# Kernel tuning notes

Hardware: AMD Instinct MI355X
Metric: run time of the kernel (lower is better)

## Reference

```python
import jax, jax.numpy as jnp
import numpy as np

NEG = -65504.0  # torch.finfo(float16).min
EPS = 1e-6

B, T, D = 2, 1024, 2048
H, HD = 16, 128          # n_head, head_dim
K = 128                  # dynamic_w_hidden_dim
IH = 1                   # dynamic_hidden_dim = H // squeeze_ratio


def _rope(x, freqs_cis):
    # x: [B,T,H,hd]; 'half' mode: first/second half are the rotation pair,
    # output is interleaved (stack(...,-1).flatten(3) in torch).
    half = x.shape[-1] // 2
    a, b = x[..., :half], x[..., half:]
    cos = freqs_cis[None, :, None, :, 0]
    sin = freqs_cis[None, :, None, :, 1]
    out = jnp.stack([a * cos - b * sin, b * cos + a * sin], axis=-1)
    return out.reshape(x.shape)


def _cross_head_proj(inputs, qw1, qw2, kw1, kw2, qdd, kdd):
    # inputs: [B,N,T,S]; qw1/qw2: [B,T,I,N]; kw1/kw2: [B,S,I,N]; qdd: [B,T,N]; kdd: [B,S,N]
    out = inputs
    out = out + jnp.einsum('bnts,btin,btim->bmts', inputs, qw1, qw2)
    out = out + jnp.einsum('bnts,bsin,bsim->bmts', inputs, kw1, kw2)
    out = out + inputs * jnp.swapaxes(qdd, 1, 2)[..., None]   # [B,N,T,1]
    out = out + inputs * jnp.swapaxes(kdd, 1, 2)[:, :, None, :]  # [B,N,1,S]
    return out


def setup_inputs() -> dict:
    key = jax.random.key(0)
    ks = jax.random.split(key, 7)
    x = jax.random.normal(ks[0], (B, T, D), jnp.float32)
    mask = jnp.tril(jnp.ones((1, 1, T, T), bool))  # causal
    # rotary tables: [T, hd/2, 2] (cos, sin)
    inv = 1.0 / (10000.0 ** (jnp.arange(0, HD, 2, dtype=jnp.float32) / HD))
    ang = jnp.arange(T, dtype=jnp.float32)[:, None] * inv[None, :]
    freqs_cis = jnp.stack([jnp.cos(ang), jnp.sin(ang)], axis=-1)
    s = 0.02
    wqkv = jax.random.normal(ks[1], (D, 3 * H * HD), jnp.float32) * s
    wo = jax.random.normal(ks[2], (H * HD, D), jnp.float32) * s
    dw1 = jax.random.normal(ks[3], (D, 4, K), jnp.float32) * s
    qkw = jax.random.normal(ks[4], (4, K, 2 * IH, H), jnp.float32) * s
    dd_w = jax.random.normal(ks[5], (D, 4 * H), jnp.float32) * s
    return {"x": x, "mask": mask, "freqs_cis": freqs_cis, "wqkv": wqkv,
            "wo": wo, "dw1": dw1, "qkw": qkw, "dd_w": dd_w}


def reference(x, mask, freqs_cis, wqkv, wo, dw1, qkw, dd_w):
    b, t, d = x.shape
    qkv = x @ wqkv
    q, k, v = jnp.split(qkv, [H * HD, 2 * H * HD], axis=-1)
    q = q.reshape(b, t, H, HD)
    k = k.reshape(b, t, H, HD)
    v = v.reshape(b, t, H, HD)
    q = _rope(q, freqs_cis)
    k = _rope(k, freqs_cis)
    q = jnp.swapaxes(q, 1, 2) * (HD ** -0.5)  # [B,H,T,hd]
    k = jnp.swapaxes(k, 1, 2)
    v = jnp.swapaxes(v, 1, 2)

    # ---- DynamicWeightProjection (G=1, squeezed) ----
    dw_hidden = jax.nn.gelu(jnp.einsum('btd,dck->btck', x, dw1), approximate=False)
    w = jnp.einsum('btck,ckim->btcim', dw_hidden, qkw)  # [B,T,4,2*IH,H]
    w1, w2 = w[..., :IH, :], w[..., IH:, :]
    w1 = w1 * jax.lax.rsqrt(jnp.mean(w1 * w1, axis=-1, keepdims=True) + EPS)
    pre_qw1, pre_kw1, post_qw1, post_kw1 = [w1[:, :, i] for i in range(4)]
    pre_qw2, pre_kw2, post_qw2, post_kw2 = [w2[:, :, i] for i in range(4)]
    dd = jnp.tanh(x @ dd_w).reshape(b, t, 4, H)
    pre_qdd, pre_kdd, post_qdd, post_kdd = [dd[:, :, i] for i in range(4)]

    # ---- attention with cross-head mixing ----
    logits = jnp.einsum('bhtd,bhsd->bhts', q, k)
    logits = _cross_head_proj(logits, pre_qw1, pre_qw2, pre_kw1, pre_kw2, pre_qdd, pre_kdd)
    logits = jnp.where(mask, logits, NEG)
    probs = jax.nn.softmax(logits, axis=-1)
    probs = _cross_head_proj(probs, post_qw1, post_qw2, post_kw1, post_kw2, post_qdd, post_kdd)
    o = jnp.einsum('bhts,bhsd->bhtd', probs, v)
    o = jnp.swapaxes(o, 1, 2).reshape(b, t, H * HD)
    return o @ wo
```

## Files before the change

kernel.cpp:

```cpp
#include <hip/hip_runtime.h>


typedef unsigned short u16;
typedef unsigned int u32;
typedef __attribute__((ext_vector_type(8))) short s16x8;
typedef __attribute__((ext_vector_type(4))) float f32x4;
typedef __attribute__((ext_vector_type(2))) float f32x2;
typedef __attribute__((ext_vector_type(2))) u16 u16x2;
typedef __attribute__((ext_vector_type(8))) u16 u16x8;

#define DEV __device__ __forceinline__

DEV float bf2f(u16 u) { union { u32 u; float f; } a; a.u = ((u32)u) << 16; return a.f; }
DEV u16 f2bf(float f) {
  union { float f; u32 u; } a; a.f = f;
  u32 r = a.u + 0x7fffu + ((a.u >> 16) & 1u);
  return (u16)(r >> 16);
}

DEV void gload16(const void* g, void* l) {
  __builtin_amdgcn_global_load_lds((__attribute__((address_space(1))) void*)g,
                                   (__attribute__((address_space(3))) void*)l,
                                   16, 0, 0);
}

template <int OUTBF>
__global__ __launch_bounds__(512, 1) void gemm256(
    const u16* __restrict__ A, const u16* __restrict__ B, void* __restrict__ Cp,
    int K, int lda, int ldb, int ldc)
{
  __shared__ u16 sA[2][256 * 64];
  __shared__ u16 sB[2][256 * 64];
  const int tid = threadIdx.x, ln = tid & 63;
  const int wid = tid >> 6, wm = wid >> 2, wn = wid & 3;

  const int nx = gridDim.x;
  const int fid = blockIdx.y * nx + blockIdx.x;
  const int cpx = (nx * gridDim.y) >> 3;
  const int nid = (fid & 7) * cpx + (fid >> 3);
  const int bx = nid % nx, by = nid / nx;

  const u16* Ab = A + (size_t)(by * 256) * lda;
  const u16* Bb = B + (size_t)(bx * 256) * ldb;

  f32x4 acc[8][4];
#pragma unroll
  for (int m = 0; m < 8; ++m)
#pragma unroll
    for (int n = 0; n < 4; ++n) {
      f32x4 zz = {0.f, 0.f, 0.f, 0.f};
      acc[m][n] = zz;
    }

  int srow[4], scol[4], soff[4];
#pragma unroll
  for (int i = 0; i < 4; ++i) {
    int o = i * 8192 + tid * 16;
    soff[i] = o;
    int r = o >> 7;
    srow[i] = r;
    scol[i] = ((o & 127) ^ ((r & 7) << 4)) >> 1;
  }

#define STAGE256(ba, bb, k0)                                              \
  {                                                                       \
    _Pragma("unroll")                                                     \
    for (int i_ = 0; i_ < 4; ++i_)                                        \
      gload16(Ab + (size_t)srow[i_] * lda + (k0) + scol[i_],              \
              (char*)(ba) + soff[i_]);                                    \
    _Pragma("unroll")                                                     \
    for (int i_ = 0; i_ < 4; ++i_)                                        \
      gload16(Bb + (size_t)srow[i_] * ldb + (k0) + scol[i_],              \
              (char*)(bb) + soff[i_]);                                    \
  }

  const int arow = wm * 128 + (ln & 15);
  const int brow = wn * 64 + (ln & 15);
  const int kb = (ln >> 4) * 16;
  const int frswz = (ln & 7) << 4;
  const int NT = K >> 6;

  STAGE256(sA[0], sB[0], 0);
  if (NT > 1) STAGE256(sA[1], sB[1], 64);

  for (int t = 0; t < NT; ++t) {
    const int c = t & 1;
    asm volatile("s_waitcnt vmcnt(8)" ::: "memory");
    __builtin_amdgcn_s_barrier();
    const char* pa = (const char*)sA[c];
    const char* pb = (const char*)sB[c];
    s16x8 bfr[4][2];
#pragma unroll
    for (int ph = 0; ph < 4; ++ph) {
      if (ph == 0) {
#pragma unroll
        for (int n = 0; n < 4; ++n)
#pragma unroll
          for (int kk = 0; kk < 2; ++kk)
            bfr[n][kk] = *(const s16x8*)(pb + (size_t)(brow + n * 16) * 128 + ((kk * 64 + kb) ^ frswz));
      }
      s16x8 afr[2][2];
#pragma unroll
      for (int mm = 0; mm < 2; ++mm)
#pragma unroll
        for (int kk = 0; kk < 2; ++kk)
          afr[mm][kk] = *(const s16x8*)(pa + (size_t)(arow + (ph * 2 + mm) * 16) * 128 + ((kk * 64 + kb) ^ frswz));
      __builtin_amdgcn_s_barrier();
      __builtin_amdgcn_s_setprio(1);
#pragma unroll
      for (int mm = 0; mm < 2; ++mm)
#pragma unroll
        for (int n = 0; n < 4; ++n)
#pragma unroll
          for (int kk = 0; kk < 2; ++kk)
            acc[ph * 2 + mm][n] = __builtin_amdgcn_mfma_f32_16x16x32_bf16(
                afr[mm][kk], bfr[n][kk], acc[ph * 2 + mm][n], 0, 0, 0);
      __builtin_amdgcn_s_setprio(0);
    }
    __builtin_amdgcn_s_barrier();
    if (t + 2 < NT) STAGE256(sA[c], sB[c], (t + 2) * 64);
  }
#undef STAGE256

  const int r0 = by * 256 + wm * 128 + ((ln >> 4) << 2);
  const int c0 = bx * 256 + wn * 64 + (ln & 15);
#pragma unroll
  for (int m = 0; m < 8; ++m)
#pragma unroll
    for (int n = 0; n < 4; ++n)
#pragma unroll
      for (int j = 0; j < 4; ++j) {
        int row = r0 + m * 16 + j, col = c0 + n * 16;
        if (OUTBF)
          ((u16*)Cp)[(size_t)row * ldc + col] = f2bf(acc[m][n][j]);
        else
          ((float*)Cp)[(size_t)row * ldc + col] = acc[m][n][j];
      }
}

template <int OUTBF>
__global__ __launch_bounds__(256) void gemm_bt(
    const u16* __restrict__ A, const u16* __restrict__ B, void* __restrict__ Cp,
    int K, int lda, int ldb, int ldc,
    long sAb, long sBb, long sCb1, long sCb2, int CZ2, int cmode, int swz)
{
  int bx = blockIdx.x, by = blockIdx.y;
  if (swz) {
    int nx = gridDim.x;
    int fid = by * nx + bx;
    int cpx = (nx * gridDim.y) >> 3;
    int nid = (fid & 7) * cpx + (fid >> 3);
    bx = nid % nx; by = nid / nx;
  }
  if (cmode == 1 && bx > by) return;
  __shared__ u16 sA[128 * 64];
  __shared__ u16 sB[128 * 64];
  const int tid = threadIdx.x, wv = tid >> 6, ln = tid & 63;
  const int z = blockIdx.z;
  const u16* Ab = A + (size_t)z * sAb + (size_t)(by * 128) * lda;
  const u16* Bb = B + (size_t)z * sBb + (size_t)(bx * 128) * ldb;
  const int wr = (wv >> 1) * 64, wc = (wv & 1) * 64;
  const int Keff = (cmode == 2) ? min(K, (by + 1) * 128) : K;

  f32x4 acc[4][4];
#pragma unroll
  for (int m = 0; m < 4; ++m)
#pragma unroll
    for (int n = 0; n < 4; ++n) {
      f32x4 zz = {0.f, 0.f, 0.f, 0.f};
      acc[m][n] = zz;
    }

  int o_[4], r_[4], cb_[4];
#pragma unroll
  for (int i = 0; i < 4; ++i) {
    int o = (wv * 4 + i) * 1024 + ln * 16;
    o_[i] = o;
    int r = o >> 7;
    r_[i] = r;
    cb_[i] = (o & 127) ^ ((r & 7) << 4);
  }
  const int frswz = (ln & 7) << 4;
  const int fkcol = (ln >> 4) << 4;

  for (int k0 = 0; k0 < Keff; k0 += 64) {
    __syncthreads();
#pragma unroll
    for (int i = 0; i < 4; ++i)
      gload16(Ab + (size_t)r_[i] * lda + (k0 + (cb_[i] >> 1)), (char*)sA + o_[i]);
#pragma unroll
    for (int i = 0; i < 4; ++i)
      gload16(Bb + (size_t)r_[i] * ldb + (k0 + (cb_[i] >> 1)), (char*)sB + o_[i]);
    __syncthreads();

#pragma unroll
    for (int ks = 0; ks < 2; ++ks) {
      s16x8 av[4], bv[4];
#pragma unroll
      for (int m = 0; m < 4; ++m) {
        int row = wr + m * 16 + (ln & 15);
        int addr = row * 128 + ((ks * 64 + fkcol) ^ frswz);
        av[m] = *(const s16x8*)((const char*)sA + addr);
      }
#pragma unroll
      for (int n = 0; n < 4; ++n) {
        int row = wc + n * 16 + (ln & 15);
        int addr = row * 128 + ((ks * 64 + fkcol) ^ frswz);
        bv[n] = *(const s16x8*)((const char*)sB + addr);
      }
#pragma unroll
      for (int m = 0; m < 4; ++m)
#pragma unroll
        for (int n = 0; n < 4; ++n)
          acc[m][n] = __builtin_amdgcn_mfma_f32_16x16x32_bf16(av[m], bv[n], acc[m][n], 0, 0, 0);
    }
  }

  const size_t cbase = (size_t)(z / CZ2) * sCb1 + (size_t)(z % CZ2) * sCb2;
  const int r0 = by * 128 + wr + ((ln >> 4) << 2);
  const int c0 = bx * 128 + wc + (ln & 15);
#pragma unroll
  for (int m = 0; m < 4; ++m)
#pragma unroll
    for (int n = 0; n < 4; ++n)
#pragma unroll
      for (int j = 0; j < 4; ++j) {
        int row = r0 + m * 16 + j, col = c0 + n * 16;
        if (OUTBF)
          ((u16*)Cp)[cbase + (size_t)row * ldc + col] = f2bf(acc[m][n][j]);
        else
          ((float*)Cp)[cbase + (size_t)row * ldc + col] = acc[m][n][j];
      }
}

template <int INBF>
__global__ __launch_bounds__(256) void transpose_to_bf16(
    const void* __restrict__ srcv, u16* __restrict__ dst,
    int R, int C, int Cpad, int srcLd, long sSrc1, long sSrc2, int Z2, long sDst)
{
  __shared__ float tile[32][33];
  const int z = blockIdx.z, z1 = z / Z2, z2 = z % Z2;
  const size_t sbase = (size_t)z1 * sSrc1 + (size_t)z2 * sSrc2;
  u16* d = dst + (size_t)z * sDst;
  const int c0 = blockIdx.x * 32, r0 = blockIdx.y * 32;
  const int tx = threadIdx.x, ty = threadIdx.y;
#pragma unroll
  for (int i = 0; i < 4; ++i) {
    int r = r0 + ty + i * 8, c = c0 + tx;
    float v = 0.f;
    if (c < C && r < R) {
      if (INBF) v = bf2f(((const u16*)srcv)[sbase + (size_t)r * srcLd + c]);
      else      v = ((const float*)srcv)[sbase + (size_t)r * srcLd + c];
    }
    tile[ty + i * 8][tx] = v;
  }
  __syncthreads();
#pragma unroll
  for (int i = 0; i < 4; ++i) {
    int dr = c0 + ty + i * 8, dc = r0 + tx;
    if (dr < Cpad && dc < R) d[(size_t)dr * R + dc] = f2bf(tile[tx][ty + i * 8]);
  }
}

__global__ void cvt_f32_bf16_k(const float* __restrict__ src, u16* __restrict__ dst, int n4) {
  int i = blockIdx.x * 256 + threadIdx.x;
  if (i >= n4) return;
  const float4 v = ((const float4*)src)[i];
  u16* o = dst + (size_t)i * 4;
  o[0] = f2bf(v.x); o[1] = f2bf(v.y); o[2] = f2bf(v.z); o[3] = f2bf(v.w);
}

__global__ __launch_bounds__(256) void rope_k(
    const u16* __restrict__ qkvm, const float* __restrict__ fc,
    u16* __restrict__ qb, u16* __restrict__ kb)
{
  const int bt = blockIdx.x, b = bt >> 10, t = bt & 1023;
  const u16* row = qkvm + (size_t)bt * 6912;
  const float SC = 0.08838834764831845f;
#pragma unroll
  for (int it = 0; it < 4; ++it) {
    int idx = threadIdx.x + it * 256;
    int h = idx >> 6, j = idx & 63;
    float c = fc[(t * 64 + j) * 2], sn = fc[(t * 64 + j) * 2 + 1];
    float qa = bf2f(row[h * 128 + j]), qbv = bf2f(row[h * 128 + 64 + j]);
    float ka = bf2f(row[2048 + h * 128 + j]), kbv = bf2f(row[2048 + h * 128 + 64 + j]);
    size_t o = ((size_t)(b * 16 + h) * 1024 + t) * 128 + 2 * j;
    qb[o]     = f2bf((qa * c - qbv * sn) * SC);
    qb[o + 1] = f2bf((qbv * c + qa * sn) * SC);
    kb[o]     = f2bf(ka * c - kbv * sn);
    kb[o + 1] = f2bf(kbv * c + ka * sn);
  }
}

__global__ __launch_bounds__(64) void gelu_bf16_k(u16* __restrict__ qm) {
  int bt = blockIdx.x, tid = threadIdx.x;
  u16* p = qm + (size_t)bt * 6912 + 6144 + tid * 8;
  u16x8 v = *(u16x8*)p;
#pragma unroll
  for (int i = 0; i < 8; ++i) {
    float f = bf2f(v[i]);
    f = 0.5f * f * (1.f + erff(f * 0.70710678118654752f));
    v[i] = f2bf(f);
  }
  *(u16x8*)p = v;
}

__global__ __launch_bounds__(64) void wproj_k(
    const u16* __restrict__ qkvm, const float* __restrict__ qkw,
    float* __restrict__ w1a, float* __restrict__ w2a, float* __restrict__ kpT)
{
  const int bt = blockIdx.x, ln = threadIdx.x;
  const int c = ln >> 4, m = ln & 15;
  const int b = bt >> 10, t = bt & 1023;
  const u16* hp = qkvm + (size_t)bt * 6912 + 6144 + c * 128;
  const float* Wp = qkw + (size_t)c * 4096 + m;
  float w1 = 0.f, w2 = 0.f;
  for (int k = 0; k < 128; ++k) {
    float hv = bf2f(hp[k]);
    w1 += hv * Wp[k * 32];
    w2 += hv * Wp[k * 32 + 16];
  }
  float ss = w1 * w1;
  ss += __shfl_xor(ss, 1); ss += __shfl_xor(ss, 2);
  ss += __shfl_xor(ss, 4); ss += __shfl_xor(ss, 8);
  float nrm = rsqrtf(ss * (1.f / 16.f) + 1e-6f);
  float w1n = w1 * nrm;
  size_t o = (size_t)bt * 64 + c * 16 + m;
  w1a[o] = w1n;
  w2a[o] = w2;
  size_t kb = (size_t)b * 98304 + (size_t)m * 1024 + t;
  if (c == 1) { kpT[kb] = w1n; kpT[kb + 16384] = w2; }
  if (c == 3) { kpT[kb + 49152] = w1n; kpT[kb + 65536] = w2; }
}

__global__ __launch_bounds__(64) void dd_k(const u16* __restrict__ qkvm,
                                           float* __restrict__ dda, float* __restrict__ kpT) {
  int bt = blockIdx.x, ln = threadIdx.x;
  int c = ln >> 4, m = ln & 15;
  int b = bt >> 10, t = bt & 1023;
  float v = tanhf(bf2f(qkvm[(size_t)bt * 6912 + 6656 + ln]));
  dda[(size_t)bt * 64 + ln] = v;
  size_t kb = (size_t)b * 98304 + (size_t)m * 1024 + t;
  if (c == 1) kpT[kb + 32768] = v;
  if (c == 3) kpT[kb + 81920] = v;
}

__global__ __launch_bounds__(512, 4) void proj_softmax_k(
    const float* __restrict__ L, u16* __restrict__ P,
    const float* __restrict__ w1a, const float* __restrict__ w2a,
    const float* __restrict__ dda, const float* __restrict__ kparT)
{
  const int t = blockIdx.x, b = blockIdx.y;
  const int tid = threadIdx.x, wv = tid >> 6, ln = tid & 63;
  const int s0 = tid * 2;
  const bool live = (s0 <= t);

  __shared__ float qpar[6][16];
  __shared__ float red2[16][8];
  __shared__ float rzf[16];
  if (tid < 96) {
    int a = tid >> 4, hh = tid & 15;
    const float* sp = (a == 0 || a == 3) ? w1a : ((a == 1 || a == 4) ? w2a : dda);
    int cc = (a < 3) ? 0 : 2;
    qpar[a][hh] = sp[(size_t)(b * 1024 + t) * 64 + cc * 16 + hh];
  }
  __syncthreads();

  const float* kp = kparT + (size_t)b * 98304 + s0;
  float v[16][2];
  const size_t lbase = ((size_t)(b * 16) * 1024 + t) * 1024 + s0;

  if (live) {
#pragma unroll
    for (int h = 0; h < 16; ++h) {
      f32x2 d = *(const f32x2*)(L + lbase + (size_t)h * 1048576);
      v[h][0] = d[0]; v[h][1] = d[1];
    }
    float dq0 = 0.f, dq1 = 0.f, dk0 = 0.f, dk1 = 0.f;
#pragma unroll
    for (int h = 0; h < 16; ++h) {
      f32x2 k1 = *(const f32x2*)(kp + h * 1024);
      dq0 += v[h][0] * qpar[0][h]; dq1 += v[h][1] * qpar[0][h];
      dk0 += v[h][0] * k1[0];      dk1 += v[h][1] * k1[1];
    }
    const bool ok1 = (s0 + 1 <= t);
#pragma unroll
    for (int h = 0; h < 16; ++h) {
      f32x2 k2 = *(const f32x2*)(kp + 16384 + h * 1024);
      f32x2 kd = *(const f32x2*)(kp + 32768 + h * 1024);
      float a0 = v[h][0] * (1.f + qpar[2][h] + kd[0]) + qpar[1][h] * dq0 + k2[0] * dk0;
      float a1 = v[h][1] * (1.f + qpar[2][h] + kd[1]) + qpar[1][h] * dq1 + k2[1] * dk1;
      v[h][0] = __expf(a0);
      v[h][1] = ok1 ? __expf(a1) : 0.f;
    }
  }

#pragma unroll
  for (int h = 0; h < 16; ++h) {
    float x = live ? (v[h][0] + v[h][1]) : 0.f;
#pragma unroll
    for (int off = 32; off > 0; off >>= 1) x += __shfl_xor(x, off);
    if (ln == 0) red2[h][wv] = x;
  }
  __syncthreads();
  if (tid < 16)
    rzf[tid] = 1.f / (((red2[tid][0] + red2[tid][1]) + (red2[tid][2] + red2[tid][3])) +
                      ((red2[tid][4] + red2[tid][5]) + (red2[tid][6] + red2[tid][7])));
  __syncthreads();

  const size_t pbase = ((size_t)(b * 16) * 1024 + t) * 1024 + s0;
  if (live) {
    float pdq0 = 0.f, pdq1 = 0.f, pdk0 = 0.f, pdk1 = 0.f;
#pragma unroll
    for (int h = 0; h < 16; ++h) {
      float rz = rzf[h];
      f32x2 k1 = *(const f32x2*)(kp + 49152 + h * 1024);
      float p0 = v[h][0] * rz, p1 = v[h][1] * rz;
      v[h][0] = p0; v[h][1] = p1;
      pdq0 += p0 * qpar[3][h]; pdq1 += p1 * qpar[3][h];
      pdk0 += p0 * k1[0];      pdk1 += p1 * k1[1];
    }
#pragma unroll
    for (int h = 0; h < 16; ++h) {
      f32x2 k2 = *(const f32x2*)(kp + 65536 + h * 1024);
      f32x2 kd = *(const f32x2*)(kp + 81920 + h * 1024);
      u16x2 pk;
      pk[0] = f2bf(v[h][0] * (1.f + qpar[5][h] + kd[0]) + qpar[4][h] * pdq0 + k2[0] * pdk0);
      pk[1] = f2bf(v[h][1] * (1.f + qpar[5][h] + kd[1]) + qpar[4][h] * pdq1 + k2[1] * pdk1);
      *(u16x2*)(P + pbase + (size_t)h * 1048576) = pk;
    }
  } else {
    u16x2 z2 = {0, 0};
#pragma unroll
    for (int h = 0; h < 16; ++h)
      *(u16x2*)(P + pbase + (size_t)h * 1048576) = z2;
  }
}

extern "C" void kernel_launch(void* const* d_in, const int* in_sizes, int n_in,
                              void* d_out, int out_size, void* d_ws, size_t ws_size,
                              hipStream_t stream)
{
  (void)in_sizes; (void)n_in; (void)out_size; (void)ws_size;
  const float* x    = (const float*)d_in[0];
  const float* fc   = (const float*)d_in[2];
  const float* wqkv = (const float*)d_in[3];
  const float* wo   = (const float*)d_in[4];
  const float* dw1  = (const float*)d_in[5];
  const float* qkw  = (const float*)d_in[6];
  const float* ddw  = (const float*)d_in[7];
  float* out = (float*)d_out;
  char* w = (char*)d_ws;

  u16*   woT   = (u16*)(w + 0);
  u16*   qb    = (u16*)(w + 8388608);
  u16*   kb    = (u16*)(w + 16777216);
  u16*   vT    = (u16*)(w + 25165824);
  u16*   obf   = (u16*)(w + 33554432);
  float* w1a   = (float*)(w + 41943040);
  float* w2a   = (float*)(w + 42467328);
  float* dda   = (float*)(w + 42991616);
  const size_t TB = 43515904;
  u16*   xb    = (u16*)(w + TB);
  u16*   wallT = (u16*)(w + TB + 8388608);
  u16*   qkvm  = (u16*)(w + TB + 36700160);
  float* L     = (float*)(w + TB);
  u16*   P     = (u16*)(w + TB + 134217728);
  float* kparT = (float*)(w + 244842496);

  cvt_f32_bf16_k<<<4096, 256, 0, stream>>>(x, xb, 1048576);
  transpose_to_bf16<0><<<dim3(192, 64, 1), dim3(32, 8), 0, stream>>>(wqkv, wallT, 2048, 6144, 6144, 6144, 0, 0, 1, 0);
  transpose_to_bf16<0><<<dim3(16, 64, 1),  dim3(32, 8), 0, stream>>>(dw1,  wallT + (size_t)6144 * 2048, 2048, 512, 512, 512, 0, 0, 1, 0);
  transpose_to_bf16<0><<<dim3(8, 64, 1),   dim3(32, 8), 0, stream>>>(ddw,  wallT + (size_t)6656 * 2048, 2048, 64, 256, 64, 0, 0, 1, 0);
  transpose_to_bf16<0><<<dim3(64, 64, 1),  dim3(32, 8), 0, stream>>>(wo,   woT, 2048, 2048, 2048, 2048, 0, 0, 1, 0);

  gemm256<1><<<dim3(27, 8, 1), 512, 0, stream>>>(xb, wallT, qkvm, 2048, 2048, 2048, 6912);
  rope_k<<<2048, 256, 0, stream>>>(qkvm, fc, qb, kb);
  transpose_to_bf16<1><<<dim3(4, 32, 32), dim3(32, 8), 0, stream>>>(qkvm + 4096, vT, 1024, 128, 128, 6912, 7077888, 128, 16, 131072);

  gelu_bf16_k<<<2048, 64, 0, stream>>>(qkvm);
  wproj_k<<<2048, 64, 0, stream>>>(qkvm, qkw, w1a, w2a, kparT);
  dd_k<<<2048, 64, 0, stream>>>(qkvm, dda, kparT);

  gemm_bt<0><<<dim3(8, 8, 32), 256, 0, stream>>>(qb, kb, L, 128, 128, 128, 1024, 131072, 131072, 1048576, 0, 1, 1, 0);
  proj_softmax_k<<<dim3(1024, 2, 1), 512, 0, stream>>>(L, P, w1a, w2a, dda, kparT);
  gemm_bt<1><<<dim3(1, 8, 32), 256, 0, stream>>>(P, vT, obf, 1024, 1024, 1024, 2048, 1048576, 131072, 2097152, 128, 16, 2, 0);

  gemm_bt<0><<<dim3(16, 16, 1), 256, 0, stream>>>(obf, woT, out, 2048, 2048, 2048, 2048, 0, 0, 0, 0, 1, 0, 1);
}
```

Before: 318.6 us.

## Store attention logits in bf16 and retile QKV GEMM to 1024 threads

The Q·K^T logits buffer now holds bf16 instead of fp32, which halves the write traffic of the logits GEMM and the read traffic of the cross-head softmax kernel. The softmax kernel converts the values back to float on load, so the logits carry less precision before the cross-head mixing and softmax. Separately, the fused QKV projection GEMM goes from 512 to 1024 threads with 16 waves, each owning a 64x64 sub-tile. Its A and B tile loads are split and staggered across phases, trading per-wave register pressure for more waves in flight.

Measured after the change: 295.2 us, median of 2. 1.08x faster.

```diff
diff --git a/kernel.cpp b/kernel.cpp
--- a/kernel.cpp
+++ b/kernel.cpp
@@ -25,7 +25,7 @@
 }
 
 template <int OUTBF>
-__global__ __launch_bounds__(512, 1) void gemm256(
+__global__ __launch_bounds__(1024, 1) void gemm256(
     const u16* __restrict__ A, const u16* __restrict__ B, void* __restrict__ Cp,
     int K, int lda, int ldb, int ldc)
 {
@@ -43,49 +43,52 @@
   const u16* Ab = A + (size_t)(by * 256) * lda;
   const u16* Bb = B + (size_t)(bx * 256) * ldb;
 
-  f32x4 acc[8][4];
-#pragma unroll
-  for (int m = 0; m < 8; ++m)
+  f32x4 acc[4][4];
+#pragma unroll
+  for (int m = 0; m < 4; ++m)
 #pragma unroll
     for (int n = 0; n < 4; ++n) {
       f32x4 zz = {0.f, 0.f, 0.f, 0.f};
       acc[m][n] = zz;
     }
 
-  int srow[4], scol[4], soff[4];
-#pragma unroll
-  for (int i = 0; i < 4; ++i) {
-    int o = i * 8192 + tid * 16;
+  int srow[2], scol[2], soff[2];
+#pragma unroll
+  for (int i = 0; i < 2; ++i) {
+    int o = i * 16384 + tid * 16;
     soff[i] = o;
     int r = o >> 7;
     srow[i] = r;
     scol[i] = ((o & 127) ^ ((r & 7) << 4)) >> 1;
   }
 
-#define STAGE256(ba, bb, k0)                                              \
+#define STAGE_A(ba, k0)                                                   \
   {                                                                       \
     _Pragma("unroll")                                                     \
-    for (int i_ = 0; i_ < 4; ++i_)                                        \
+    for (int i_ = 0; i_ < 2; ++i_)                                        \
       gload16(Ab + (size_t)srow[i_] * lda + (k0) + scol[i_],              \
               (char*)(ba) + soff[i_]);                                    \
+  }
+#define STAGE_B(bb, k0)                                                   \
+  {                                                                       \
     _Pragma("unroll")                                                     \
-    for (int i_ = 0; i_ < 4; ++i_)                                        \
+    for (int i_ = 0; i_ < 2; ++i_)                                        \
       gload16(Bb + (size_t)srow[i_] * ldb + (k0) + scol[i_],              \
               (char*)(bb) + soff[i_]);                                    \
   }
 
-  const int arow = wm * 128 + (ln & 15);
+  const int arow = wm * 64 + (ln & 15);
   const int brow = wn * 64 + (ln & 15);
   const int kb = (ln >> 4) * 16;
   const int frswz = (ln & 7) << 4;
   const int NT = K >> 6;
 
-  STAGE256(sA[0], sB[0], 0);
-  if (NT > 1) STAGE256(sA[1], sB[1], 64);
+  STAGE_A(sA[0], 0); STAGE_B(sB[0], 0);
+  STAGE_A(sA[1], 64); STAGE_B(sB[1], 64);
 
   for (int t = 0; t < NT; ++t) {
     const int c = t & 1;
-    asm volatile("s_waitcnt vmcnt(8)" ::: "memory");
+    asm volatile("s_waitcnt vmcnt(4)" ::: "memory");
     __builtin_amdgcn_s_barrier();
     const char* pa = (const char*)sA[c];
     const char* pb = (const char*)sB[c];
@@ -99,33 +102,31 @@
           for (int kk = 0; kk < 2; ++kk)
             bfr[n][kk] = *(const s16x8*)(pb + (size_t)(brow + n * 16) * 128 + ((kk * 64 + kb) ^ frswz));
       }
-      s16x8 afr[2][2];
-#pragma unroll
-      for (int mm = 0; mm < 2; ++mm)
+      s16x8 afr[2];
+#pragma unroll
+      for (int kk = 0; kk < 2; ++kk)
+        afr[kk] = *(const s16x8*)(pa + (size_t)(arow + ph * 16) * 128 + ((kk * 64 + kb) ^ frswz));
+      __builtin_amdgcn_s_barrier();
+      if (ph == 1 && t + 2 < NT) STAGE_B(sB[c], (t + 2) * 64);
+      __builtin_amdgcn_s_setprio(1);
+#pragma unroll
+      for (int n = 0; n < 4; ++n)
 #pragma unroll
         for (int kk = 0; kk < 2; ++kk)
-          afr[mm][kk] = *(const s16x8*)(pa + (size_t)(arow + (ph * 2 + mm) * 16) * 128 + ((kk * 64 + kb) ^ frswz));
-      __builtin_amdgcn_s_barrier();
-      __builtin_amdgcn_s_setprio(1);
-#pragma unroll
-      for (int mm = 0; mm < 2; ++mm)
-#pragma unroll
-        for (int n = 0; n < 4; ++n)
-#pragma unroll
-          for (int kk = 0; kk < 2; ++kk)
-            acc[ph * 2 + mm][n] = __builtin_amdgcn_mfma_f32_16x16x32_bf16(
-                afr[mm][kk], bfr[n][kk], acc[ph * 2 + mm][n], 0, 0, 0);
+          acc[ph][n] = __builtin_amdgcn_mfma_f32_16x16x32_bf16(
+              afr[kk], bfr[n][kk], acc[ph][n], 0, 0, 0);
       __builtin_amdgcn_s_setprio(0);
     }
     __builtin_amdgcn_s_barrier();
-    if (t + 2 < NT) STAGE256(sA[c], sB[c], (t + 2) * 64);
-  }
-#undef STAGE256
-
-  const int r0 = by * 256 + wm * 128 + ((ln >> 4) << 2);
+    if (t + 2 < NT) STAGE_A(sA[c], (t + 2) * 64);
+  }
+#undef STAGE_A
+#undef STAGE_B
+
+  const int r0 = by * 256 + wm * 64 + ((ln >> 4) << 2);
   const int c0 = bx * 256 + wn * 64 + (ln & 15);
 #pragma unroll
-  for (int m = 0; m < 8; ++m)
+  for (int m = 0; m < 4; ++m)
 #pragma unroll
     for (int n = 0; n < 4; ++n)
 #pragma unroll
@@ -346,7 +347,7 @@
 }
 
 __global__ __launch_bounds__(512, 4) void proj_softmax_k(
-    const float* __restrict__ L, u16* __restrict__ P,
+    const u16* __restrict__ L, u16* __restrict__ P,
     const float* __restrict__ w1a, const float* __restrict__ w2a,
     const float* __restrict__ dda, const float* __restrict__ kparT)
 {
@@ -373,8 +374,8 @@
   if (live) {
 #pragma unroll
     for (int h = 0; h < 16; ++h) {
-      f32x2 d = *(const f32x2*)(L + lbase + (size_t)h * 1048576);
-      v[h][0] = d[0]; v[h][1] = d[1];
+      u16x2 d = *(const u16x2*)(L + lbase + (size_t)h * 1048576);
+      v[h][0] = bf2f(d[0]); v[h][1] = bf2f(d[1]);
     }
     float dq0 = 0.f, dq1 = 0.f, dk0 = 0.f, dk1 = 0.f;
 #pragma unroll
@@ -464,8 +465,8 @@
   u16*   xb    = (u16*)(w + TB);
   u16*   wallT = (u16*)(w + TB + 8388608);
   u16*   qkvm  = (u16*)(w + TB + 36700160);
-  float* L     = (float*)(w + TB);
-  u16*   P     = (u16*)(w + TB + 134217728);
+  u16*   L     = (u16*)(w + TB);
+  u16*   P     = (u16*)(w + TB + 67108864);
   float* kparT = (float*)(w + 244842496);
 
   cvt_f32_bf16_k<<<4096, 256, 0, stream>>>(x, xb, 1048576);
@@ -474,7 +475,7 @@
   transpose_to_bf16<0><<<dim3(8, 64, 1),   dim3(32, 8), 0, stream>>>(ddw,  wallT + (size_t)6656 * 2048, 2048, 64, 256, 64, 0, 0, 1, 0);
   transpose_to_bf16<0><<<dim3(64, 64, 1),  dim3(32, 8), 0, stream>>>(wo,   woT, 2048, 2048, 2048, 2048, 0, 0, 1, 0);
 
-  gemm256<1><<<dim3(27, 8, 1), 512, 0, stream>>>(xb, wallT, qkvm, 2048, 2048, 2048, 6912);
+  gemm256<1><<<dim3(27, 8, 1), 1024, 0, stream>>>(xb, wallT, qkvm, 2048, 2048, 2048, 6912);
   rope_k<<<2048, 256, 0, stream>>>(qkvm, fc, qb, kb);
   transpose_to_bf16<1><<<dim3(4, 32, 32), dim3(32, 8), 0, stream>>>(qkvm + 4096, vT, 1024, 128, 128, 6912, 7077888, 128, 16, 131072);
 
@@ -482,7 +483,7 @@
   wproj_k<<<2048, 64, 0, stream>>>(qkvm, qkw, w1a, w2a, kparT);
   dd_k<<<2048, 64, 0, stream>>>(qkvm, dda, kparT);
 
-  gemm_bt<0><<<dim3(8, 8, 32), 256, 0, stream>>>(qb, kb, L, 128, 128, 128, 1024, 131072, 131072, 1048576, 0, 1, 1, 0);
+  gemm_bt<1><<<dim3(8, 8, 32), 256, 0, stream>>>(qb, kb, L, 128, 128, 128, 1024, 131072, 131072, 1048576, 0, 1, 1, 0);
   proj_softmax_k<<<dim3(1024, 2, 1), 512, 0, stream>>>(L, P, w1a, w2a, dda, kparT);
   gemm_bt<1><<<dim3(1, 8, 32), 256, 0, stream>>>(P, vT, obf, 1024, 1024, 1024, 2048, 1048576, 131072, 2097152, 128, 16, 2, 0);
 
```
